# Kernel optimization log

Measured on AMD Instinct MI355X. Metric: run time of the kernel, lower is better.

The kernel has to match this reference:

```python
import jax, jax.numpy as jnp
import numpy as np

D = 1024

def setup_inputs() -> dict:
    key = jax.random.key(0)
    ks = jax.random.split(key, 9)
    B, S = 4, 2048
    s = 1.0 / np.sqrt(D)
    return {
        "query": jax.random.normal(ks[0], (B, S, D), jnp.float32),
        "key": jax.random.normal(ks[1], (B, S, D), jnp.float32),
        "value": jax.random.normal(ks[2], (B, S, D), jnp.float32),
        "Wq": jax.random.normal(ks[3], (D, D), jnp.float32) * s,
        "bq": jax.random.normal(ks[4], (D,), jnp.float32) * 0.01,
        "Wk": jax.random.normal(ks[5], (D, D), jnp.float32) * s,
        "bk": jax.random.normal(ks[6], (D,), jnp.float32) * 0.01,
        "Wv": jax.random.normal(ks[7], (D, D), jnp.float32) * s,
        "bv": jax.random.normal(ks[8], (D,), jnp.float32) * 0.01,
    }

def reference(query, key, value, Wq, bq, Wk, bk, Wv, bv):
    scale = 1.0 / (query.shape[-1] ** 0.5)
    q = jnp.einsum('bsd,ed->bse', query, Wq) + bq  # nn.Linear: x @ W.T + b
    k = jnp.einsum('bsd,ed->bse', key, Wk) + bk
    v = jnp.einsum('bsd,ed->bse', value, Wv) + bv
    scores = jnp.einsum('bqd,bkd->bqk', q, k) * scale  # [B, Sq, Skv]
    w = jax.nn.softmax(scores, axis=-1)
    return jnp.einsum('bqk,bkd->bqd', w, v)
```

## Files before the change

### kernel.cpp

```cpp
#include <hip/hip_runtime.h>

typedef __bf16 bf16x8 __attribute__((ext_vector_type(8)));
typedef float f32x4 __attribute__((ext_vector_type(4)));
typedef unsigned short u16x8 __attribute__((ext_vector_type(8)));

__device__ inline unsigned short f2bf(float f) {
  union { float f; unsigned u; } a; a.f = f;
  return (unsigned short)((a.u + 0x7fffu + ((a.u >> 16) & 1u)) >> 16);
}
__device__ inline float bf2f(unsigned short h) {
  union { unsigned u; float f; } a; a.u = ((unsigned)h) << 16;
  return a.f;
}

struct CvtArgs {
  const float* src[6];
  unsigned short* dst[6];
};

__global__ __launch_bounds__(256) void cvt6(CvtArgs a) {
  long long i = (long long)blockIdx.x * 256 + threadIdx.x;
  int idx; long long off;
  if (i < 6291456LL) { idx = (int)(i >> 21); off = i & ((1LL << 21) - 1); }
  else { long long j = i - 6291456LL; idx = 3 + (int)(j >> 18); off = j & ((1LL << 18) - 1); }
  float4 v = ((const float4*)a.src[idx])[off];
  ushort4 o;
  o.x = f2bf(v.x); o.y = f2bf(v.y); o.z = f2bf(v.z); o.w = f2bf(v.w);
  ((ushort4*)a.dst[idx])[off] = o;
}

#define EPI_PROJ 0
#define EPI_SCALE 1
#define EPI_OUT 2

struct GP {
  const unsigned short* A;
  const unsigned short* B;
  unsigned short* C;
  unsigned short* outQ; unsigned short* outK; unsigned short* outV;
  const float* biasQ; const float* biasK; const float* biasV;
  long long batchA, batchB, batchC;
  int lda, ldb, ldc, K;
  float scale;
};

#define G2L(gp, lp) __builtin_amdgcn_global_load_lds( \
    (const __attribute__((address_space(1))) void*)(gp), \
    (__attribute__((address_space(3))) void*)(lp), 16, 0, 0)

#define MFMA_(d, a, b) d = __builtin_amdgcn_mfma_f32_16x16x32_bf16(a, b, d, 0, 0, 0)
#define SB0() __builtin_amdgcn_sched_barrier(0)
#define LGKM(n) do { asm volatile("s_waitcnt lgkmcnt(" #n ")" ::: "memory"); SB0(); } while (0)
#define VMC(n) do { asm volatile("s_waitcnt vmcnt(" #n ")" ::: "memory"); SB0(); } while (0)

template<int BM, int BN, int WMW, int WNW, int EPI>
__global__ __launch_bounds__(512, 2) void gemm2(GP p) {
  constexpr int WAVES_N = BN / WNW;
  constexpr int AMF = WMW / 16;
  constexpr int BNF = WNW / 16;
  constexpr int AH = AMF / 2, BH = BNF / 2;
  constexpr int AF_N = AH * 2;
  constexpr int NBA = BM / 64, NBB = BN / 64;
  static_assert((BM / WMW) * WAVES_N == 8, "8 waves");
  static_assert(BNF == 4, "lgkm immediates assume BNF==4");

  extern __shared__ char smem[];
  char* smA = smem;
  char* smB = smem + 2 * BM * 128;

  const int tid = threadIdx.x;
  const int lane = tid & 63;
  const int wid = tid >> 6;
  const int wm = wid / WAVES_N, wn = wid % WAVES_N;

  const int gx = gridDim.x, gy = gridDim.y;
  const int nwg = gx * gy * (int)gridDim.z;
  int orig = blockIdx.x + gx * (blockIdx.y + gy * blockIdx.z);
  int qq = nwg >> 3, rr_ = nwg & 7;
  int xcd = orig & 7, sl = orig >> 3;
  int wg = (xcd < rr_ ? xcd * (qq + 1) : rr_ * (qq + 1) + (xcd - rr_) * qq) + sl;
  int bx = wg % gx;
  int t2 = wg / gx;
  int by = t2 % gy;
  int z  = t2 / gy;

  const int m0 = by * BM, n0 = bx * BN;

  const long long lda2 = (long long)p.lda * 2;
  const long long ldb2 = (long long)p.ldb * 2;
  const char* Abase = (const char*)(p.A + (long long)z * p.batchA) + (long long)m0 * lda2;
  const char* Bbase = (const char*)(p.B + (long long)z * p.batchB) + (long long)n0 * ldb2;

  const int trow = tid >> 3;
  const int cs = (((tid & 7) ^ (trow & 7)) << 4);
  const char* srcA = Abase + (long long)trow * lda2 + cs;
  const char* srcB = Bbase + (long long)trow * ldb2 + cs;

  const int NT = p.K >> 6;

  const int aRowB = ((wm * WMW + (lane & 15)) << 7);
  const int bRowB = ((wn * WNW + (lane & 15)) << 7);
  const int csw = (lane & 7) << 4;
  const int ck0 = (((lane >> 4) << 4)) ^ csw;
  const int ck1 = ((((lane >> 4) << 4)) | 64) ^ csw;

  f32x4 acc[AMF][BNF];
#pragma unroll
  for (int i = 0; i < AMF; ++i)
#pragma unroll
    for (int j = 0; j < BNF; ++j) acc[i][j] = (f32x4){0.f, 0.f, 0.f, 0.f};

  bf16x8 aLo[AH][2], aHi[AH][2], bLo[BH][2], bHi[BH][2];

  auto stage = [&](int t) {
    char* dA = smA + (t & 1) * (BM * 128) + (tid << 4);
    char* dB = smB + (t & 1) * (BN * 128) + (tid << 4);
    const char* sA = srcA + (long long)t * 128;
    const char* sB = srcB + (long long)t * 128;
#pragma unroll
    for (int c = 0; c < NBA; ++c) G2L(sA + (long long)c * (lda2 << 6), dA + c * 8192);
#pragma unroll
    for (int c = 0; c < NBB; ++c) G2L(sB + (long long)c * (ldb2 << 6), dB + c * 8192);
  };
  auto readAh = [&](int t, int half, bf16x8 (&dst)[AH][2]) {
    const char* ra = smA + (t & 1) * (BM * 128) + aRowB + half * (AH * 2048);
#pragma unroll
    for (int mi = 0; mi < AH; ++mi) {
      dst[mi][0] = *(const bf16x8*)(ra + mi * 2048 + ck0);
      dst[mi][1] = *(const bf16x8*)(ra + mi * 2048 + ck1);
    }
  };
  auto readBh = [&](int t, int half, bf16x8 (&dst)[BH][2]) {
    const char* rb = smB + (t & 1) * (BN * 128) + bRowB + half * (BH * 2048);
#pragma unroll
    for (int ni = 0; ni < BH; ++ni) {
      dst[ni][0] = *(const bf16x8*)(rb + ni * 2048 + ck0);
      dst[ni][1] = *(const bf16x8*)(rb + ni * 2048 + ck1);
    }
  };
  auto quad = [&](int qa, int qb, bf16x8 (&A)[AH][2], bf16x8 (&B)[BH][2]) {
    __builtin_amdgcn_s_setprio(1);
#pragma unroll
    for (int mi = 0; mi < AH; ++mi)
#pragma unroll
      for (int ni = 0; ni < BH; ++ni) {
        MFMA_(acc[qa * AH + mi][qb * BH + ni], A[mi][0], B[ni][0]);
        MFMA_(acc[qa * AH + mi][qb * BH + ni], A[mi][1], B[ni][1]);
      }
    __builtin_amdgcn_s_setprio(0);
  };

  stage(0); stage(1);
  if constexpr (NBA + NBB == 8) VMC(8); else VMC(6);
  __builtin_amdgcn_s_barrier();
  readAh(0, 0, aLo); readBh(0, 0, bLo);
  SB0();

  for (int t = 0; t < NT; ++t) {
    readAh(t, 1, aHi);
    SB0();
    if constexpr (AF_N == 8) LGKM(8); else LGKM(4);
    quad(0, 0, aLo, bLo);
    readBh(t, 1, bHi);
    SB0();
    LGKM(4);
    quad(1, 0, aHi, bLo);
    LGKM(0);
    quad(0, 1, aLo, bHi);
    quad(1, 1, aHi, bHi);
    VMC(0);
    __builtin_amdgcn_s_barrier();
    if (t + 2 < NT) stage(t + 2);
    if (t + 1 < NT) { readAh(t + 1, 0, aLo); readBh(t + 1, 0, bLo); }
    SB0();
  }

  const int c0 = lane & 15;
  const int r0 = (lane >> 4) << 2;
  if constexpr (EPI == EPI_SCALE) {
    unsigned short* Cz = p.C + (long long)z * p.batchC;
#pragma unroll
    for (int mi = 0; mi < AMF; ++mi) {
      const int grow = m0 + wm * WMW + (mi << 4) + r0;
#pragma unroll
      for (int ni = 0; ni < BNF; ++ni) {
        const int gcol = n0 + wn * WNW + (ni << 4) + c0;
#pragma unroll
        for (int rr = 0; rr < 4; ++rr)
          Cz[(long long)(grow + rr) * p.ldc + gcol] = f2bf(acc[mi][ni][rr] * p.scale);
      }
    }
  } else if constexpr (EPI == EPI_OUT) {
    float* Cz = (float*)p.C + (long long)z * p.batchC;
#pragma unroll
    for (int mi = 0; mi < AMF; ++mi) {
      const int grow = m0 + wm * WMW + (mi << 4) + r0;
#pragma unroll
      for (int ni = 0; ni < BNF; ++ni) {
        const int gcol = n0 + wn * WNW + (ni << 4) + c0;
#pragma unroll
        for (int rr = 0; rr < 4; ++rr)
          Cz[(long long)(grow + rr) * p.ldc + gcol] = acc[mi][ni][rr] * p.scale;
      }
    }
  } else {
    if (z < 2) {
      unsigned short* O = (z == 0) ? p.outQ : p.outK;
      const float* bias = (z == 0) ? p.biasQ : p.biasK;
#pragma unroll
      for (int mi = 0; mi < AMF; ++mi) {
        const int grow = m0 + wm * WMW + (mi << 4) + r0;
#pragma unroll
        for (int ni = 0; ni < BNF; ++ni) {
          const int gcol = n0 + wn * WNW + (ni << 4) + c0;
          const float bb = bias[gcol];
#pragma unroll
          for (int rr = 0; rr < 4; ++rr)
            O[(long long)(grow + rr) * 1024 + gcol] = f2bf(acc[mi][ni][rr] + bb);
        }
      }
    } else {
#pragma unroll
      for (int mi = 0; mi < AMF; ++mi) {
        const int grow = m0 + wm * WMW + (mi << 4) + r0;
        const int bb = grow >> 11, s = grow & 2047;
#pragma unroll
        for (int ni = 0; ni < BNF; ++ni) {
          const int d = n0 + wn * WNW + (ni << 4) + c0;
          const float ba = p.biasV[d];
          ushort4 pk;
          pk.x = f2bf(acc[mi][ni][0] + ba);
          pk.y = f2bf(acc[mi][ni][1] + ba);
          pk.z = f2bf(acc[mi][ni][2] + ba);
          pk.w = f2bf(acc[mi][ni][3] + ba);
          *(ushort4*)(p.outV + ((long long)bb << 21) + (long long)d * 2048 + s) = pk;
        }
      }
    }
  }
}

__global__ __launch_bounds__(256) void softmax_rows(unsigned short* __restrict__ S) {
  const size_t row = blockIdx.x;
  unsigned short* pp = S + row * 2048;
  const int t = threadIdx.x, lane = t & 63, wave = t >> 6;
  u16x8 h = ((const u16x8*)pp)[t];
  float x[8];
#pragma unroll
  for (int j = 0; j < 8; ++j) x[j] = bf2f(h[j]);
  float m = x[0];
#pragma unroll
  for (int j = 1; j < 8; ++j) m = fmaxf(m, x[j]);
#pragma unroll
  for (int off = 32; off >= 1; off >>= 1) m = fmaxf(m, __shfl_xor(m, off, 64));
  __shared__ float rmax[4], rsum[4];
  if (lane == 0) rmax[wave] = m;
  __syncthreads();
  m = fmaxf(fmaxf(rmax[0], rmax[1]), fmaxf(rmax[2], rmax[3]));
  float e[8], sum = 0.f;
#pragma unroll
  for (int j = 0; j < 8; ++j) { e[j] = __expf(x[j] - m); sum += e[j]; }
#pragma unroll
  for (int off = 32; off >= 1; off >>= 1) sum += __shfl_xor(sum, off, 64);
  if (lane == 0) rsum[wave] = sum;
  __syncthreads();
  sum = rsum[0] + rsum[1] + rsum[2] + rsum[3];
  const float inv = 1.f / sum;
  u16x8 o;
#pragma unroll
  for (int j = 0; j < 8; ++j) o[j] = f2bf(e[j] * inv);
  ((u16x8*)pp)[t] = o;
}

extern "C" void kernel_launch(void* const* d_in, const int* in_sizes, int n_in,
                              void* d_out, int out_size, void* d_ws, size_t ws_size,
                              hipStream_t stream) {
  const float* q  = (const float*)d_in[0];
  const float* k  = (const float*)d_in[1];
  const float* v  = (const float*)d_in[2];
  const float* Wq = (const float*)d_in[3];
  const float* bq = (const float*)d_in[4];
  const float* Wk = (const float*)d_in[5];
  const float* bk = (const float*)d_in[6];
  const float* Wv = (const float*)d_in[7];
  const float* bv = (const float*)d_in[8];

  unsigned short* Xb = (unsigned short*)d_ws;
  unsigned short* Wb = Xb + 25165824;
  unsigned short* qb = Wb + 3145728;
  unsigned short* kb = qb + 8388608;
  unsigned short* vT = kb + 8388608;
  unsigned short* S  = Xb;

  (void)hipFuncSetAttribute((const void*)gemm2<256,256,128,64,EPI_PROJ>,
      hipFuncAttributeMaxDynamicSharedMemorySize, 131072);
  (void)hipFuncSetAttribute((const void*)gemm2<256,256,128,64,EPI_SCALE>,
      hipFuncAttributeMaxDynamicSharedMemorySize, 131072);
  (void)hipFuncSetAttribute((const void*)gemm2<256,128,64,64,EPI_OUT>,
      hipFuncAttributeMaxDynamicSharedMemorySize, 98304);

  CvtArgs ca;
  ca.src[0] = q;  ca.src[1] = k;  ca.src[2] = v;
  ca.src[3] = Wq; ca.src[4] = Wk; ca.src[5] = Wv;
  ca.dst[0] = Xb;            ca.dst[1] = Xb + 8388608; ca.dst[2] = Xb + 16777216;
  ca.dst[3] = Wb;            ca.dst[4] = Wb + 1048576; ca.dst[5] = Wb + 2097152;
  cvt6<<<27648, 256, 0, stream>>>(ca);

  GP gp{};
  gp.A = Xb;  gp.batchA = 8388608; gp.lda = 1024;
  gp.B = Wb;  gp.batchB = 1048576; gp.ldb = 1024;
  gp.outQ = qb; gp.outK = kb; gp.outV = vT;
  gp.biasQ = bq; gp.biasK = bk; gp.biasV = bv;
  gp.K = 1024; gp.scale = 1.f;
  gemm2<256,256,128,64,EPI_PROJ><<<dim3(4, 32, 3), 512, 131072, stream>>>(gp);

  GP gs{};
  gs.A = qb; gs.batchA = 2097152; gs.lda = 1024;
  gs.B = kb; gs.batchB = 2097152; gs.ldb = 1024;
  gs.C = S;  gs.batchC = 4194304; gs.ldc = 2048;
  gs.K = 1024; gs.scale = 0.03125f;
  gemm2<256,256,128,64,EPI_SCALE><<<dim3(8, 8, 4), 512, 131072, stream>>>(gs);

  softmax_rows<<<8192, 256, 0, stream>>>(S);

  GP gv{};
  gv.A = S;  gv.batchA = 4194304; gv.lda = 2048;
  gv.B = vT; gv.batchB = 2097152; gv.ldb = 2048;
  gv.C = (unsigned short*)d_out; gv.batchC = 2097152; gv.ldc = 1024;
  gv.K = 2048; gv.scale = 1.f;
  gemm2<256,128,64,64,EPI_OUT><<<dim3(8, 8, 4), 512, 98304, stream>>>(gv);
}
```

Baseline: 183.2 us.

## Add K=32 tile variant and use 128x128 tiles for projection and PV GEMMs

Adds a KT template parameter so the GEMM can stage 32-wide K slices, with a new swizzled LDS layout that packs two rows per 128-byte line, plus 4-wave 256-thread blocks. The QKV projection and the PV GEMM switch from 256-wide 8-wave tiles to 128x128 tiles with KT=32, using 32 KB of shared memory and more workgroups. The aim is higher occupancy and better CU fill on the smaller grids. In exchange, each tile reuses less data, each K step has fewer MFMAs per barrier, and the new layout's wait-count immediates have to be right.

```diff
diff --git a/kernel.cpp b/kernel.cpp
--- a/kernel.cpp
+++ b/kernel.cpp
@@ -53,25 +53,28 @@
 #define LGKM(n) do { asm volatile("s_waitcnt lgkmcnt(" #n ")" ::: "memory"); SB0(); } while (0)
 #define VMC(n) do { asm volatile("s_waitcnt vmcnt(" #n ")" ::: "memory"); SB0(); } while (0)
 
-template<int BM, int BN, int WMW, int WNW, int EPI>
-__global__ __launch_bounds__(512, 2) void gemm2(GP p) {
-  constexpr int WAVES_N = BN / WNW;
-  constexpr int AMF = WMW / 16;
-  constexpr int BNF = WNW / 16;
+template<int BM, int BN, int WMW, int WNW, int KT, int EPI>
+__global__ __launch_bounds__((BM/WMW)*(BN/WNW)*64, ((BM/WMW)*(BN/WNW) == 8) ? 2 : 4)
+void gemm2(GP p) {
+  constexpr int NWN = BN / WNW;
+  constexpr int THREADS = (BM / WMW) * NWN * 64;
+  constexpr int AMF = WMW / 16, BNF = WNW / 16;
   constexpr int AH = AMF / 2, BH = BNF / 2;
-  constexpr int AF_N = AH * 2;
-  constexpr int NBA = BM / 64, NBB = BN / 64;
-  static_assert((BM / WMW) * WAVES_N == 8, "8 waves");
-  static_assert(BNF == 4, "lgkm immediates assume BNF==4");
+  constexpr int KTB = KT * 2;
+  constexpr int ABUF = BM * KTB, BBUF = BN * KTB;
+  constexpr int CHUNK = THREADS * 16;
+  constexpr int NBA = ABUF / CHUNK, NBB = BBUF / CHUNK;
+  static_assert(BNF == 4 && BH == 2, "wave shape");
+  static_assert(KT == 64 || (AH == 2), "KT32 only for 64-wide wave M");
 
   extern __shared__ char smem[];
   char* smA = smem;
-  char* smB = smem + 2 * BM * 128;
+  char* smB = smem + 2 * ABUF;
 
   const int tid = threadIdx.x;
   const int lane = tid & 63;
   const int wid = tid >> 6;
-  const int wm = wid / WAVES_N, wn = wid % WAVES_N;
+  const int wm = wid / NWN, wn = wid % NWN;
 
   const int gx = gridDim.x, gy = gridDim.y;
   const int nwg = gx * gy * (int)gridDim.z;
@@ -91,18 +94,37 @@
   const char* Abase = (const char*)(p.A + (long long)z * p.batchA) + (long long)m0 * lda2;
   const char* Bbase = (const char*)(p.B + (long long)z * p.batchB) + (long long)n0 * ldb2;
 
-  const int trow = tid >> 3;
-  const int cs = (((tid & 7) ^ (trow & 7)) << 4);
-  const char* srcA = Abase + (long long)trow * lda2 + cs;
-  const char* srcB = Bbase + (long long)trow * ldb2 + cs;
-
-  const int NT = p.K >> 6;
-
-  const int aRowB = ((wm * WMW + (lane & 15)) << 7);
-  const int bRowB = ((wn * WNW + (lane & 15)) << 7);
-  const int csw = (lane & 7) << 4;
-  const int ck0 = (((lane >> 4) << 4)) ^ csw;
-  const int ck1 = ((((lane >> 4) << 4)) | 64) ^ csw;
+  const char* srcA; const char* srcB;
+  if constexpr (KT == 64) {
+    const int trow = tid >> 3;
+    const int cs = (((tid & 7) ^ (trow & 7)) << 4);
+    srcA = Abase + (long long)trow * lda2 + cs;
+    srcB = Bbase + (long long)trow * ldb2 + cs;
+  } else {
+    const int line = tid >> 3, s = tid & 7;
+    const int sg = s ^ (line & 7);
+    const int srow = 2 * line + (sg >> 2);
+    const int scol = (sg & 3) << 4;
+    srcA = Abase + (long long)srow * lda2 + scol;
+    srcB = Bbase + (long long)srow * ldb2 + scol;
+  }
+
+  const int NT = p.K / KT;
+
+  int aOff, bOff, ck0 = 0, ck1 = 0;
+  if constexpr (KT == 64) {
+    aOff = ((wm * WMW + (lane & 15)) << 7);
+    bOff = ((wn * WNW + (lane & 15)) << 7);
+    const int csw = (lane & 7) << 4;
+    ck0 = (((lane >> 4) << 4)) ^ csw;
+    ck1 = ((((lane >> 4) << 4)) | 64) ^ csw;
+  } else {
+    const int kh = lane >> 4;
+    const int Ra = wm * WMW + (lane & 15);
+    const int Rb = wn * WNW + (lane & 15);
+    aOff = ((Ra >> 1) << 7) + (((((Ra & 1) << 2) | kh) ^ ((Ra >> 1) & 7)) << 4);
+    bOff = ((Rb >> 1) << 7) + (((((Rb & 1) << 2) | kh) ^ ((Rb >> 1) & 7)) << 4);
+  }
 
   f32x4 acc[AMF][BNF];
 #pragma unroll
@@ -113,29 +135,37 @@
   bf16x8 aLo[AH][2], aHi[AH][2], bLo[BH][2], bHi[BH][2];
 
   auto stage = [&](int t) {
-    char* dA = smA + (t & 1) * (BM * 128) + (tid << 4);
-    char* dB = smB + (t & 1) * (BN * 128) + (tid << 4);
-    const char* sA = srcA + (long long)t * 128;
-    const char* sB = srcB + (long long)t * 128;
-#pragma unroll
-    for (int c = 0; c < NBA; ++c) G2L(sA + (long long)c * (lda2 << 6), dA + c * 8192);
-#pragma unroll
-    for (int c = 0; c < NBB; ++c) G2L(sB + (long long)c * (ldb2 << 6), dB + c * 8192);
+    char* dA = smA + (t & 1) * ABUF + (tid << 4);
+    char* dB = smB + (t & 1) * BBUF + (tid << 4);
+    const char* sA = srcA + (long long)t * KTB;
+    const char* sB = srcB + (long long)t * KTB;
+#pragma unroll
+    for (int c = 0; c < NBA; ++c) G2L(sA + (long long)c * 64 * lda2, dA + c * CHUNK);
+#pragma unroll
+    for (int c = 0; c < NBB; ++c) G2L(sB + (long long)c * 64 * ldb2, dB + c * CHUNK);
   };
   auto readAh = [&](int t, int half, bf16x8 (&dst)[AH][2]) {
-    const char* ra = smA + (t & 1) * (BM * 128) + aRowB + half * (AH * 2048);
+    const char* ra = smA + (t & 1) * ABUF;
 #pragma unroll
     for (int mi = 0; mi < AH; ++mi) {
-      dst[mi][0] = *(const bf16x8*)(ra + mi * 2048 + ck0);
-      dst[mi][1] = *(const bf16x8*)(ra + mi * 2048 + ck1);
+      if constexpr (KT == 64) {
+        dst[mi][0] = *(const bf16x8*)(ra + aOff + ((half * AH + mi) << 11) + ck0);
+        dst[mi][1] = *(const bf16x8*)(ra + aOff + ((half * AH + mi) << 11) + ck1);
+      } else {
+        dst[mi][0] = *(const bf16x8*)(ra + aOff + (half * AH + mi) * 1024);
+      }
     }
   };
   auto readBh = [&](int t, int half, bf16x8 (&dst)[BH][2]) {
-    const char* rb = smB + (t & 1) * (BN * 128) + bRowB + half * (BH * 2048);
+    const char* rb = smB + (t & 1) * BBUF;
 #pragma unroll
     for (int ni = 0; ni < BH; ++ni) {
-      dst[ni][0] = *(const bf16x8*)(rb + ni * 2048 + ck0);
-      dst[ni][1] = *(const bf16x8*)(rb + ni * 2048 + ck1);
+      if constexpr (KT == 64) {
+        dst[ni][0] = *(const bf16x8*)(rb + bOff + ((half * BH + ni) << 11) + ck0);
+        dst[ni][1] = *(const bf16x8*)(rb + bOff + ((half * BH + ni) << 11) + ck1);
+      } else {
+        dst[ni][0] = *(const bf16x8*)(rb + bOff + (half * BH + ni) * 1024);
+      }
     }
   };
   auto quad = [&](int qa, int qb, bf16x8 (&A)[AH][2], bf16x8 (&B)[BH][2]) {
@@ -145,13 +175,14 @@
 #pragma unroll
       for (int ni = 0; ni < BH; ++ni) {
         MFMA_(acc[qa * AH + mi][qb * BH + ni], A[mi][0], B[ni][0]);
-        MFMA_(acc[qa * AH + mi][qb * BH + ni], A[mi][1], B[ni][1]);
+        if constexpr (KT == 64)
+          MFMA_(acc[qa * AH + mi][qb * BH + ni], A[mi][1], B[ni][1]);
       }
     __builtin_amdgcn_s_setprio(0);
   };
 
   stage(0); stage(1);
-  if constexpr (NBA + NBB == 8) VMC(8); else VMC(6);
+  if constexpr (NBA + NBB == 8) VMC(8); else VMC(4);
   __builtin_amdgcn_s_barrier();
   readAh(0, 0, aLo); readBh(0, 0, bLo);
   SB0();
@@ -159,11 +190,12 @@
   for (int t = 0; t < NT; ++t) {
     readAh(t, 1, aHi);
     SB0();
-    if constexpr (AF_N == 8) LGKM(8); else LGKM(4);
+    if constexpr (KT == 64) { if constexpr (AH == 4) LGKM(8); else LGKM(4); }
+    else LGKM(2);
     quad(0, 0, aLo, bLo);
     readBh(t, 1, bHi);
     SB0();
-    LGKM(4);
+    if constexpr (KT == 64) LGKM(4); else LGKM(2);
     quad(1, 0, aHi, bLo);
     LGKM(0);
     quad(0, 1, aLo, bHi);
@@ -292,12 +324,12 @@
   unsigned short* vT = kb + 8388608;
   unsigned short* S  = Xb;
 
-  (void)hipFuncSetAttribute((const void*)gemm2<256,256,128,64,EPI_PROJ>,
+  (void)hipFuncSetAttribute((const void*)gemm2<128,128,64,64,32,EPI_PROJ>,
+      hipFuncAttributeMaxDynamicSharedMemorySize, 32768);
+  (void)hipFuncSetAttribute((const void*)gemm2<256,256,128,64,64,EPI_SCALE>,
       hipFuncAttributeMaxDynamicSharedMemorySize, 131072);
-  (void)hipFuncSetAttribute((const void*)gemm2<256,256,128,64,EPI_SCALE>,
-      hipFuncAttributeMaxDynamicSharedMemorySize, 131072);
-  (void)hipFuncSetAttribute((const void*)gemm2<256,128,64,64,EPI_OUT>,
-      hipFuncAttributeMaxDynamicSharedMemorySize, 98304);
+  (void)hipFuncSetAttribute((const void*)gemm2<128,128,64,64,32,EPI_OUT>,
+      hipFuncAttributeMaxDynamicSharedMemorySize, 32768);
 
   CvtArgs ca;
   ca.src[0] = q;  ca.src[1] = k;  ca.src[2] = v;
@@ -312,14 +344,14 @@
   gp.outQ = qb; gp.outK = kb; gp.outV = vT;
   gp.biasQ = bq; gp.biasK = bk; gp.biasV = bv;
   gp.K = 1024; gp.scale = 1.f;
-  gemm2<256,256,128,64,EPI_PROJ><<<dim3(4, 32, 3), 512, 131072, stream>>>(gp);
+  gemm2<128,128,64,64,32,EPI_PROJ><<<dim3(8, 64, 3), 256, 32768, stream>>>(gp);
 
   GP gs{};
   gs.A = qb; gs.batchA = 2097152; gs.lda = 1024;
   gs.B = kb; gs.batchB = 2097152; gs.ldb = 1024;
   gs.C = S;  gs.batchC = 4194304; gs.ldc = 2048;
   gs.K = 1024; gs.scale = 0.03125f;
-  gemm2<256,256,128,64,EPI_SCALE><<<dim3(8, 8, 4), 512, 131072, stream>>>(gs);
+  gemm2<256,256,128,64,64,EPI_SCALE><<<dim3(8, 8, 4), 512, 131072, stream>>>(gs);
 
   softmax_rows<<<8192, 256, 0, stream>>>(S);
 
@@ -328,5 +360,5 @@
   gv.B = vT; gv.batchB = 2097152; gv.ldb = 2048;
   gv.C = (unsigned short*)d_out; gv.batchC = 2097152; gv.ldc = 1024;
   gv.K = 2048; gv.scale = 1.f;
-  gemm2<256,128,64,64,EPI_OUT><<<dim3(8, 8, 4), 512, 98304, stream>>>(gv);
-}
+  gemm2<128,128,64,64,32,EPI_OUT><<<dim3(8, 16, 4), 256, 32768, stream>>>(gv);
+}
```

Result: no change. 185.1 us (+1.0%).

## Switch GEMM to triple-buffered BK=32 pipeline with issue-ahead staging

Applied to the files above, without the earlier changes.

Rewrites the GEMM mainloop to use a K-step of 32 instead of 64, with three rotating LDS buffers. Global-to-LDS loads for tile t+2 are issued at the top of each iteration, and only the previous stage is waited on, so memory latency overlaps the MFMAs instead of draining with vmcnt(0) every step. The LDS layout is repacked two rows per 128-byte line with a new XOR swizzle. The projection GEMM moves to 256x128 tiles with a larger grid, and launch bounds now allow up to 4 blocks per CU via a reduced shared-memory footprint. The costs are twice as many loop iterations and barriers per K, and extra register pressure under the higher occupancy target.

```diff
diff --git a/kernel.cpp b/kernel.cpp
--- a/kernel.cpp
+++ b/kernel.cpp
@@ -53,25 +53,25 @@
 #define LGKM(n) do { asm volatile("s_waitcnt lgkmcnt(" #n ")" ::: "memory"); SB0(); } while (0)
 #define VMC(n) do { asm volatile("s_waitcnt vmcnt(" #n ")" ::: "memory"); SB0(); } while (0)
 
-template<int BM, int BN, int WMW, int WNW, int EPI>
-__global__ __launch_bounds__(512, 2) void gemm2(GP p) {
-  constexpr int WAVES_N = BN / WNW;
-  constexpr int AMF = WMW / 16;
-  constexpr int BNF = WNW / 16;
+template<int BM, int BN, int WMW, int WNW, int MINW, int EPI>
+__global__ __launch_bounds__(512, MINW) void gemm3(GP p) {
+  constexpr int NWN = BN / WNW;
+  constexpr int AMF = WMW / 16, BNF = WNW / 16;
   constexpr int AH = AMF / 2, BH = BNF / 2;
-  constexpr int AF_N = AH * 2;
-  constexpr int NBA = BM / 64, NBB = BN / 64;
-  static_assert((BM / WMW) * WAVES_N == 8, "8 waves");
-  static_assert(BNF == 4, "lgkm immediates assume BNF==4");
+  constexpr int ABUF = BM * 64, BBUF = BN * 64;
+  constexpr int NBA = ABUF / 8192, NBB = BBUF / 8192;
+  static_assert((BM / WMW) * NWN == 8, "8 waves");
+  static_assert(BNF == 4, "BH==2 assumed");
+  static_assert(NBA >= 1 && NBB >= 1, "chunking");
 
   extern __shared__ char smem[];
   char* smA = smem;
-  char* smB = smem + 2 * BM * 128;
+  char* smB = smem + 3 * ABUF;
 
   const int tid = threadIdx.x;
   const int lane = tid & 63;
   const int wid = tid >> 6;
-  const int wm = wid / WAVES_N, wn = wid % WAVES_N;
+  const int wm = wid / NWN, wn = wid % NWN;
 
   const int gx = gridDim.x, gy = gridDim.y;
   const int nwg = gx * gy * (int)gridDim.z;
@@ -91,18 +91,20 @@
   const char* Abase = (const char*)(p.A + (long long)z * p.batchA) + (long long)m0 * lda2;
   const char* Bbase = (const char*)(p.B + (long long)z * p.batchB) + (long long)n0 * ldb2;
 
-  const int trow = tid >> 3;
-  const int cs = (((tid & 7) ^ (trow & 7)) << 4);
-  const char* srcA = Abase + (long long)trow * lda2 + cs;
-  const char* srcB = Bbase + (long long)trow * ldb2 + cs;
-
-  const int NT = p.K >> 6;
-
-  const int aRowB = ((wm * WMW + (lane & 15)) << 7);
-  const int bRowB = ((wn * WNW + (lane & 15)) << 7);
-  const int csw = (lane & 7) << 4;
-  const int ck0 = (((lane >> 4) << 4)) ^ csw;
-  const int ck1 = ((((lane >> 4) << 4)) | 64) ^ csw;
+  const int line = tid >> 3;
+  const int sg = (tid & 7) ^ (line & 7);
+  const long long srowA = 2 * line + (sg >> 2);
+  const int scol = (sg & 3) << 4;
+  const char* srcA = Abase + srowA * lda2 + scol;
+  const char* srcB = Bbase + srowA * ldb2 + scol;
+
+  const int NT = p.K >> 5;
+
+  const int kh = lane >> 4;
+  const int Ra = wm * WMW + (lane & 15);
+  const int Rb = wn * WNW + (lane & 15);
+  const int aOff = ((Ra >> 1) << 7) + (((((Ra & 1) << 2) | kh) ^ ((Ra >> 1) & 7)) << 4);
+  const int bOff = ((Rb >> 1) << 7) + (((((Rb & 1) << 2) | kh) ^ ((Rb >> 1) & 7)) << 4);
 
   f32x4 acc[AMF][BNF];
 #pragma unroll
@@ -110,69 +112,69 @@
 #pragma unroll
     for (int j = 0; j < BNF; ++j) acc[i][j] = (f32x4){0.f, 0.f, 0.f, 0.f};
 
-  bf16x8 aLo[AH][2], aHi[AH][2], bLo[BH][2], bHi[BH][2];
-
-  auto stage = [&](int t) {
-    char* dA = smA + (t & 1) * (BM * 128) + (tid << 4);
-    char* dB = smB + (t & 1) * (BN * 128) + (tid << 4);
-    const char* sA = srcA + (long long)t * 128;
-    const char* sB = srcB + (long long)t * 128;
-#pragma unroll
-    for (int c = 0; c < NBA; ++c) G2L(sA + (long long)c * (lda2 << 6), dA + c * 8192);
-#pragma unroll
-    for (int c = 0; c < NBB; ++c) G2L(sB + (long long)c * (ldb2 << 6), dB + c * 8192);
+  bf16x8 aLo[AH], aHi[AH], bLo[BH], bHi[BH];
+
+  auto stage = [&](int t, int b) {
+    char* dA = smA + b * ABUF + (tid << 4);
+    char* dB = smB + b * BBUF + (tid << 4);
+    const char* sA = srcA + (long long)t * 64;
+    const char* sB = srcB + (long long)t * 64;
+#pragma unroll
+    for (int c = 0; c < NBA; ++c) G2L(sA + (long long)c * 128 * lda2, dA + c * 8192);
+#pragma unroll
+    for (int c = 0; c < NBB; ++c) G2L(sB + (long long)c * 128 * ldb2, dB + c * 8192);
   };
-  auto readAh = [&](int t, int half, bf16x8 (&dst)[AH][2]) {
-    const char* ra = smA + (t & 1) * (BM * 128) + aRowB + half * (AH * 2048);
-#pragma unroll
-    for (int mi = 0; mi < AH; ++mi) {
-      dst[mi][0] = *(const bf16x8*)(ra + mi * 2048 + ck0);
-      dst[mi][1] = *(const bf16x8*)(ra + mi * 2048 + ck1);
-    }
+  auto readAh = [&](int b, int half, bf16x8 (&dst)[AH]) {
+    const char* ra = smA + b * ABUF + aOff + half * (AH << 10);
+#pragma unroll
+    for (int mi = 0; mi < AH; ++mi)
+      dst[mi] = *(const bf16x8*)(ra + (mi << 10));
   };
-  auto readBh = [&](int t, int half, bf16x8 (&dst)[BH][2]) {
-    const char* rb = smB + (t & 1) * (BN * 128) + bRowB + half * (BH * 2048);
-#pragma unroll
-    for (int ni = 0; ni < BH; ++ni) {
-      dst[ni][0] = *(const bf16x8*)(rb + ni * 2048 + ck0);
-      dst[ni][1] = *(const bf16x8*)(rb + ni * 2048 + ck1);
-    }
+  auto readBh = [&](int b, int half, bf16x8 (&dst)[BH]) {
+    const char* rb = smB + b * BBUF + bOff + half * (BH << 10);
+#pragma unroll
+    for (int ni = 0; ni < BH; ++ni)
+      dst[ni] = *(const bf16x8*)(rb + (ni << 10));
   };
-  auto quad = [&](int qa, int qb, bf16x8 (&A)[AH][2], bf16x8 (&B)[BH][2]) {
+  auto quad = [&](int qa, int qb, bf16x8 (&A)[AH], bf16x8 (&B)[BH]) {
     __builtin_amdgcn_s_setprio(1);
 #pragma unroll
     for (int mi = 0; mi < AH; ++mi)
 #pragma unroll
-      for (int ni = 0; ni < BH; ++ni) {
-        MFMA_(acc[qa * AH + mi][qb * BH + ni], A[mi][0], B[ni][0]);
-        MFMA_(acc[qa * AH + mi][qb * BH + ni], A[mi][1], B[ni][1]);
-      }
+      for (int ni = 0; ni < BH; ++ni)
+        MFMA_(acc[qa * AH + mi][qb * BH + ni], A[mi], B[ni]);
     __builtin_amdgcn_s_setprio(0);
   };
 
-  stage(0); stage(1);
-  if constexpr (NBA + NBB == 8) VMC(8); else VMC(6);
+  stage(0, 0); stage(1, 1);
+  if constexpr (NBA + NBB == 4) VMC(4); else VMC(3);
   __builtin_amdgcn_s_barrier();
   readAh(0, 0, aLo); readBh(0, 0, bLo);
   SB0();
 
+  int b0 = 0, b1 = 1, b2 = 2;
   for (int t = 0; t < NT; ++t) {
-    readAh(t, 1, aHi);
-    SB0();
-    if constexpr (AF_N == 8) LGKM(8); else LGKM(4);
-    quad(0, 0, aLo, bLo);
-    readBh(t, 1, bHi);
+    if (t + 2 < NT) stage(t + 2, b2);
+    readAh(b0, 1, aHi);
     SB0();
     LGKM(4);
+    quad(0, 0, aLo, bLo);
+    readBh(b0, 1, bHi);
+    SB0();
+    LGKM(2);
     quad(1, 0, aHi, bLo);
     LGKM(0);
     quad(0, 1, aLo, bHi);
     quad(1, 1, aHi, bHi);
-    VMC(0);
+    if (t + 2 < NT) {
+      if constexpr (NBA + NBB == 4) VMC(4); else VMC(3);
+    } else {
+      VMC(0);
+    }
     __builtin_amdgcn_s_barrier();
-    if (t + 2 < NT) stage(t + 2);
-    if (t + 1 < NT) { readAh(t + 1, 0, aLo); readBh(t + 1, 0, bLo); }
+    if (t + 1 < NT) { readAh(b1, 0, aLo); readBh(b1, 0, bLo); }
     SB0();
+    int tmp = b0; b0 = b1; b1 = b2; b2 = tmp;
   }
 
   const int c0 = lane & 15;
@@ -292,12 +294,12 @@
   unsigned short* vT = kb + 8388608;
   unsigned short* S  = Xb;
 
-  (void)hipFuncSetAttribute((const void*)gemm2<256,256,128,64,EPI_PROJ>,
-      hipFuncAttributeMaxDynamicSharedMemorySize, 131072);
-  (void)hipFuncSetAttribute((const void*)gemm2<256,256,128,64,EPI_SCALE>,
-      hipFuncAttributeMaxDynamicSharedMemorySize, 131072);
-  (void)hipFuncSetAttribute((const void*)gemm2<256,128,64,64,EPI_OUT>,
+  (void)hipFuncSetAttribute((const void*)gemm3<256,128,64,64,4,EPI_PROJ>,
+      hipFuncAttributeMaxDynamicSharedMemorySize, 73728);
+  (void)hipFuncSetAttribute((const void*)gemm3<256,256,128,64,2,EPI_SCALE>,
       hipFuncAttributeMaxDynamicSharedMemorySize, 98304);
+  (void)hipFuncSetAttribute((const void*)gemm3<256,128,64,64,2,EPI_OUT>,
+      hipFuncAttributeMaxDynamicSharedMemorySize, 73728);
 
   CvtArgs ca;
   ca.src[0] = q;  ca.src[1] = k;  ca.src[2] = v;
@@ -312,14 +314,14 @@
   gp.outQ = qb; gp.outK = kb; gp.outV = vT;
   gp.biasQ = bq; gp.biasK = bk; gp.biasV = bv;
   gp.K = 1024; gp.scale = 1.f;
-  gemm2<256,256,128,64,EPI_PROJ><<<dim3(4, 32, 3), 512, 131072, stream>>>(gp);
+  gemm3<256,128,64,64,4,EPI_PROJ><<<dim3(8, 32, 3), 512, 73728, stream>>>(gp);
 
   GP gs{};
   gs.A = qb; gs.batchA = 2097152; gs.lda = 1024;
   gs.B = kb; gs.batchB = 2097152; gs.ldb = 1024;
   gs.C = S;  gs.batchC = 4194304; gs.ldc = 2048;
   gs.K = 1024; gs.scale = 0.03125f;
-  gemm2<256,256,128,64,EPI_SCALE><<<dim3(8, 8, 4), 512, 131072, stream>>>(gs);
+  gemm3<256,256,128,64,2,EPI_SCALE><<<dim3(8, 8, 4), 512, 98304, stream>>>(gs);
 
   softmax_rows<<<8192, 256, 0, stream>>>(S);
 
@@ -328,5 +330,5 @@
   gv.B = vT; gv.batchB = 2097152; gv.ldb = 2048;
   gv.C = (unsigned short*)d_out; gv.batchC = 2097152; gv.ldc = 1024;
   gv.K = 2048; gv.scale = 1.f;
-  gemm2<256,128,64,64,EPI_OUT><<<dim3(8, 8, 4), 512, 98304, stream>>>(gv);
-}
+  gemm3<256,128,64,64,2,EPI_OUT><<<dim3(8, 8, 4), 512, 73728, stream>>>(gv);
+}
```

After: 182.9 us. About the same (-0.2%).

## Fuse fp32-to-bf16 activation conversion into projection GEMM loads

Applied to the files above, without the earlier changes.

Drops the separate pass that converted the query, key and value activations to bf16. A new projection GEMM loads the fp32 activations straight into shared memory and converts them to bf16 in registers before the MFMA, with a 256x128 tile. Only the weights are still pre-converted by a small kernel. This removes a full read-write round trip over the large activation tensors, at the cost of twice the shared-memory and LDS-read traffic for A and extra conversion instructions in the inner loop.

```diff
diff --git a/kernel.cpp b/kernel.cpp
--- a/kernel.cpp
+++ b/kernel.cpp
@@ -13,23 +13,180 @@
   return a.f;
 }
 
-struct CvtArgs {
-  const float* src[6];
-  unsigned short* dst[6];
-};
-
-__global__ __launch_bounds__(256) void cvt6(CvtArgs a) {
-  long long i = (long long)blockIdx.x * 256 + threadIdx.x;
-  int idx; long long off;
-  if (i < 6291456LL) { idx = (int)(i >> 21); off = i & ((1LL << 21) - 1); }
-  else { long long j = i - 6291456LL; idx = 3 + (int)(j >> 18); off = j & ((1LL << 18) - 1); }
-  float4 v = ((const float4*)a.src[idx])[off];
+__global__ __launch_bounds__(256) void cvtW(const float* __restrict__ Wq,
+                                            const float* __restrict__ Wk,
+                                            const float* __restrict__ Wv,
+                                            unsigned short* __restrict__ Wb) {
+  int i = blockIdx.x * 256 + threadIdx.x;
+  int idx = i >> 18;
+  int off = i & 262143;
+  const float* s = (idx == 0) ? Wq : ((idx == 1) ? Wk : Wv);
+  float4 v = ((const float4*)s)[off];
   ushort4 o;
   o.x = f2bf(v.x); o.y = f2bf(v.y); o.z = f2bf(v.z); o.w = f2bf(v.w);
-  ((ushort4*)a.dst[idx])[off] = o;
-}
-
-#define EPI_PROJ 0
+  ((ushort4*)(Wb + idx * 1048576))[off] = o;
+}
+
+#define G2L(gp, lp) __builtin_amdgcn_global_load_lds( \
+    (const __attribute__((address_space(1))) void*)(gp), \
+    (__attribute__((address_space(3))) void*)(lp), 16, 0, 0)
+
+#define MFMA_(d, a, b) d = __builtin_amdgcn_mfma_f32_16x16x32_bf16(a, b, d, 0, 0, 0)
+#define SB0() __builtin_amdgcn_sched_barrier(0)
+#define LGKM(n) do { asm volatile("s_waitcnt lgkmcnt(" #n ")" ::: "memory"); SB0(); } while (0)
+#define VMC(n) do { asm volatile("s_waitcnt vmcnt(" #n ")" ::: "memory"); SB0(); } while (0)
+
+struct PJ {
+  const float* A0; const float* A1; const float* A2;
+  const unsigned short* B;
+  unsigned short* outQ; unsigned short* outK; unsigned short* outV;
+  const float* biasQ; const float* biasK; const float* biasV;
+};
+
+__global__ __launch_bounds__(512, 2) void gemmP(PJ p) {
+  extern __shared__ char smem[];
+  char* smA = smem;
+  char* smB = smem + 65536;
+  const int tid = threadIdx.x, lane = tid & 63, wid = tid >> 6;
+  const int wm = wid >> 1, wn = wid & 1;
+
+  int orig = blockIdx.x + 8 * (blockIdx.y + 32 * blockIdx.z);
+  int wg = (orig & 7) * 96 + (orig >> 3);
+  int bx = wg & 7; int t2 = wg >> 3; int by = t2 & 31; int z = t2 >> 5;
+  const int m0 = by << 8, n0 = bx << 7;
+
+  const float* Az = (z == 0) ? p.A0 : ((z == 1) ? p.A1 : p.A2);
+
+  const int lineT = tid >> 3;
+  const int sg = (tid & 7) ^ (lineT & 7);
+  const char* srcA = (const char*)(Az + (long long)(m0 + lineT) * 1024) + (sg << 4);
+  const int srowB = 2 * lineT + (sg >> 2);
+  const char* srcB = (const char*)(p.B + (long long)z * 1048576
+                                   + (long long)(n0 + srowB) * 1024) + ((sg & 3) << 4);
+
+  const int aBase = (((wm << 6) + (lane & 15)) << 7);
+  const int ax = lane & 7;
+  const int ck0 = ((((lane >> 4) << 1) | 0) ^ ax) << 4;
+  const int ck1 = ((((lane >> 4) << 1) | 1) ^ ax) << 4;
+  const int rb2 = (lane & 15) >> 1;
+  const int bBase = ((wn << 5) + rb2) << 7;
+  const int bX = ((((lane & 1) << 2) | (lane >> 4)) ^ rb2) << 4;
+
+  f32x4 acc[4][4];
+#pragma unroll
+  for (int i = 0; i < 4; ++i)
+#pragma unroll
+    for (int j = 0; j < 4; ++j) acc[i][j] = (f32x4){0.f, 0.f, 0.f, 0.f};
+
+  f32x4 aLoF[2][2], aHiF[2][2];
+  bf16x8 aLoB[2], aHiB[2], bLo[2], bHi[2];
+
+  auto stage = [&](int t) {
+    char* dA = smA + ((t & 1) << 15) + (tid << 4);
+    char* dB = smB + ((t & 1) << 13) + (tid << 4);
+    const char* sA = srcA + (long long)t * 128;
+#pragma unroll
+    for (int c = 0; c < 4; ++c) G2L(sA + ((long long)c << 18), dA + (c << 13));
+    G2L(srcB + (long long)t * 64, dB);
+  };
+  auto readA = [&](int b, int half, f32x4 (&dst)[2][2]) {
+    const char* ra = smA + (b << 15) + aBase + (half << 12);
+#pragma unroll
+    for (int f = 0; f < 2; ++f) {
+      dst[f][0] = *(const f32x4*)(ra + (f << 11) + ck0);
+      dst[f][1] = *(const f32x4*)(ra + (f << 11) + ck1);
+    }
+  };
+  auto readB = [&](int b, int half, bf16x8 (&dst)[2]) {
+    const char* rb = smB + (b << 13) + bBase + (half << 11);
+#pragma unroll
+    for (int f = 0; f < 2; ++f)
+      dst[f] = *(const bf16x8*)(rb + (f << 10) + bX);
+  };
+  auto cvtA = [&](f32x4 (&s)[2][2], bf16x8 (&d)[2]) {
+#pragma unroll
+    for (int f = 0; f < 2; ++f)
+      d[f] = (bf16x8){(__bf16)s[f][0][0], (__bf16)s[f][0][1],
+                      (__bf16)s[f][0][2], (__bf16)s[f][0][3],
+                      (__bf16)s[f][1][0], (__bf16)s[f][1][1],
+                      (__bf16)s[f][1][2], (__bf16)s[f][1][3]};
+  };
+  auto quadP = [&](int qa, int qb, bf16x8 (&A)[2], bf16x8 (&B)[2]) {
+    __builtin_amdgcn_s_setprio(1);
+#pragma unroll
+    for (int mi = 0; mi < 2; ++mi)
+#pragma unroll
+      for (int ni = 0; ni < 2; ++ni)
+        MFMA_(acc[qa * 2 + mi][qb * 2 + ni], A[mi], B[ni]);
+    __builtin_amdgcn_s_setprio(0);
+  };
+
+  stage(0);
+  VMC(0);
+  __builtin_amdgcn_s_barrier();
+  readA(0, 0, aLoF); readB(0, 0, bLo);
+  SB0();
+
+  const int NT = 32;
+  for (int t = 0; t < NT; ++t) {
+    if (t + 1 < NT) stage(t + 1);
+    SB0();
+    LGKM(2);
+    cvtA(aLoF, aLoB);
+    readA(t & 1, 1, aHiF);
+    SB0();
+    LGKM(4);
+    quadP(0, 0, aLoB, bLo);
+    readB(t & 1, 1, bHi);
+    SB0();
+    LGKM(2);
+    cvtA(aHiF, aHiB);
+    quadP(1, 0, aHiB, bLo);
+    LGKM(0);
+    quadP(0, 1, aLoB, bHi);
+    quadP(1, 1, aHiB, bHi);
+    VMC(0);
+    __builtin_amdgcn_s_barrier();
+    if (t + 1 < NT) { readA((t + 1) & 1, 0, aLoF); readB((t + 1) & 1, 0, bLo); }
+    SB0();
+  }
+
+  const int c0 = lane & 15, r0 = (lane >> 4) << 2;
+  if (z < 2) {
+    unsigned short* O = (z == 0) ? p.outQ : p.outK;
+    const float* bias = (z == 0) ? p.biasQ : p.biasK;
+#pragma unroll
+    for (int mi = 0; mi < 4; ++mi) {
+      const int grow = m0 + (wm << 6) + (mi << 4) + r0;
+#pragma unroll
+      for (int ni = 0; ni < 4; ++ni) {
+        const int gcol = n0 + (wn << 6) + (ni << 4) + c0;
+        const float bb = bias[gcol];
+#pragma unroll
+        for (int rr = 0; rr < 4; ++rr)
+          O[(long long)(grow + rr) * 1024 + gcol] = f2bf(acc[mi][ni][rr] + bb);
+      }
+    }
+  } else {
+#pragma unroll
+    for (int mi = 0; mi < 4; ++mi) {
+      const int grow = m0 + (wm << 6) + (mi << 4) + r0;
+      const int bb = grow >> 11, s = grow & 2047;
+#pragma unroll
+      for (int ni = 0; ni < 4; ++ni) {
+        const int d = n0 + (wn << 6) + (ni << 4) + c0;
+        const float ba = p.biasV[d];
+        ushort4 pk;
+        pk.x = f2bf(acc[mi][ni][0] + ba);
+        pk.y = f2bf(acc[mi][ni][1] + ba);
+        pk.z = f2bf(acc[mi][ni][2] + ba);
+        pk.w = f2bf(acc[mi][ni][3] + ba);
+        *(ushort4*)(p.outV + ((long long)bb << 21) + (long long)d * 2048 + s) = pk;
+      }
+    }
+  }
+}
+
 #define EPI_SCALE 1
 #define EPI_OUT 2
 
@@ -37,31 +194,19 @@
   const unsigned short* A;
   const unsigned short* B;
   unsigned short* C;
-  unsigned short* outQ; unsigned short* outK; unsigned short* outV;
-  const float* biasQ; const float* biasK; const float* biasV;
   long long batchA, batchB, batchC;
   int lda, ldb, ldc, K;
   float scale;
 };
 
-#define G2L(gp, lp) __builtin_amdgcn_global_load_lds( \
-    (const __attribute__((address_space(1))) void*)(gp), \
-    (__attribute__((address_space(3))) void*)(lp), 16, 0, 0)
-
-#define MFMA_(d, a, b) d = __builtin_amdgcn_mfma_f32_16x16x32_bf16(a, b, d, 0, 0, 0)
-#define SB0() __builtin_amdgcn_sched_barrier(0)
-#define LGKM(n) do { asm volatile("s_waitcnt lgkmcnt(" #n ")" ::: "memory"); SB0(); } while (0)
-#define VMC(n) do { asm volatile("s_waitcnt vmcnt(" #n ")" ::: "memory"); SB0(); } while (0)
-
 template<int BM, int BN, int WMW, int WNW, int EPI>
 __global__ __launch_bounds__(512, 2) void gemm2(GP p) {
-  constexpr int WAVES_N = BN / WNW;
-  constexpr int AMF = WMW / 16;
-  constexpr int BNF = WNW / 16;
+  constexpr int NWN = BN / WNW;
+  constexpr int AMF = WMW / 16, BNF = WNW / 16;
   constexpr int AH = AMF / 2, BH = BNF / 2;
   constexpr int AF_N = AH * 2;
   constexpr int NBA = BM / 64, NBB = BN / 64;
-  static_assert((BM / WMW) * WAVES_N == 8, "8 waves");
+  static_assert((BM / WMW) * NWN == 8, "8 waves");
   static_assert(BNF == 4, "lgkm immediates assume BNF==4");
 
   extern __shared__ char smem[];
@@ -71,7 +216,7 @@
   const int tid = threadIdx.x;
   const int lane = tid & 63;
   const int wid = tid >> 6;
-  const int wm = wid / WAVES_N, wn = wid % WAVES_N;
+  const int wm = wid / NWN, wn = wid % NWN;
 
   const int gx = gridDim.x, gy = gridDim.y;
   const int nwg = gx * gy * (int)gridDim.z;
@@ -190,7 +335,7 @@
           Cz[(long long)(grow + rr) * p.ldc + gcol] = f2bf(acc[mi][ni][rr] * p.scale);
       }
     }
-  } else if constexpr (EPI == EPI_OUT) {
+  } else {
     float* Cz = (float*)p.C + (long long)z * p.batchC;
 #pragma unroll
     for (int mi = 0; mi < AMF; ++mi) {
@@ -201,40 +346,6 @@
 #pragma unroll
         for (int rr = 0; rr < 4; ++rr)
           Cz[(long long)(grow + rr) * p.ldc + gcol] = acc[mi][ni][rr] * p.scale;
-      }
-    }
-  } else {
-    if (z < 2) {
-      unsigned short* O = (z == 0) ? p.outQ : p.outK;
-      const float* bias = (z == 0) ? p.biasQ : p.biasK;
-#pragma unroll
-      for (int mi = 0; mi < AMF; ++mi) {
-        const int grow = m0 + wm * WMW + (mi << 4) + r0;
-#pragma unroll
-        for (int ni = 0; ni < BNF; ++ni) {
-          const int gcol = n0 + wn * WNW + (ni << 4) + c0;
-          const float bb = bias[gcol];
-#pragma unroll
-          for (int rr = 0; rr < 4; ++rr)
-            O[(long long)(grow + rr) * 1024 + gcol] = f2bf(acc[mi][ni][rr] + bb);
-        }
-      }
-    } else {
-#pragma unroll
-      for (int mi = 0; mi < AMF; ++mi) {
-        const int grow = m0 + wm * WMW + (mi << 4) + r0;
-        const int bb = grow >> 11, s = grow & 2047;
-#pragma unroll
-        for (int ni = 0; ni < BNF; ++ni) {
-          const int d = n0 + wn * WNW + (ni << 4) + c0;
-          const float ba = p.biasV[d];
-          ushort4 pk;
-          pk.x = f2bf(acc[mi][ni][0] + ba);
-          pk.y = f2bf(acc[mi][ni][1] + ba);
-          pk.z = f2bf(acc[mi][ni][2] + ba);
-          pk.w = f2bf(acc[mi][ni][3] + ba);
-          *(ushort4*)(p.outV + ((long long)bb << 21) + (long long)d * 2048 + s) = pk;
-        }
       }
     }
   }
@@ -285,34 +396,27 @@
   const float* Wv = (const float*)d_in[7];
   const float* bv = (const float*)d_in[8];
 
-  unsigned short* Xb = (unsigned short*)d_ws;
-  unsigned short* Wb = Xb + 25165824;
+  unsigned short* S  = (unsigned short*)d_ws;
+  unsigned short* Wb = S + 16777216;
   unsigned short* qb = Wb + 3145728;
   unsigned short* kb = qb + 8388608;
   unsigned short* vT = kb + 8388608;
-  unsigned short* S  = Xb;
-
-  (void)hipFuncSetAttribute((const void*)gemm2<256,256,128,64,EPI_PROJ>,
-      hipFuncAttributeMaxDynamicSharedMemorySize, 131072);
+
+  (void)hipFuncSetAttribute((const void*)gemmP,
+      hipFuncAttributeMaxDynamicSharedMemorySize, 81920);
   (void)hipFuncSetAttribute((const void*)gemm2<256,256,128,64,EPI_SCALE>,
       hipFuncAttributeMaxDynamicSharedMemorySize, 131072);
   (void)hipFuncSetAttribute((const void*)gemm2<256,128,64,64,EPI_OUT>,
       hipFuncAttributeMaxDynamicSharedMemorySize, 98304);
 
-  CvtArgs ca;
-  ca.src[0] = q;  ca.src[1] = k;  ca.src[2] = v;
-  ca.src[3] = Wq; ca.src[4] = Wk; ca.src[5] = Wv;
-  ca.dst[0] = Xb;            ca.dst[1] = Xb + 8388608; ca.dst[2] = Xb + 16777216;
-  ca.dst[3] = Wb;            ca.dst[4] = Wb + 1048576; ca.dst[5] = Wb + 2097152;
-  cvt6<<<27648, 256, 0, stream>>>(ca);
-
-  GP gp{};
-  gp.A = Xb;  gp.batchA = 8388608; gp.lda = 1024;
-  gp.B = Wb;  gp.batchB = 1048576; gp.ldb = 1024;
-  gp.outQ = qb; gp.outK = kb; gp.outV = vT;
-  gp.biasQ = bq; gp.biasK = bk; gp.biasV = bv;
-  gp.K = 1024; gp.scale = 1.f;
-  gemm2<256,256,128,64,EPI_PROJ><<<dim3(4, 32, 3), 512, 131072, stream>>>(gp);
+  cvtW<<<3072, 256, 0, stream>>>(Wq, Wk, Wv, Wb);
+
+  PJ pj{};
+  pj.A0 = q; pj.A1 = k; pj.A2 = v;
+  pj.B = Wb;
+  pj.outQ = qb; pj.outK = kb; pj.outV = vT;
+  pj.biasQ = bq; pj.biasK = bk; pj.biasV = bv;
+  gemmP<<<dim3(8, 32, 3), 512, 81920, stream>>>(pj);
 
   GP gs{};
   gs.A = qb; gs.batchA = 2097152; gs.lda = 1024;
```

Result: faster. 166.9 us (-8.9%).
